# Optimization experiments

Measured on AMD Instinct MI355X. Metric: run time of the kernel, lower is better.

## Reference

```python
import jax, jax.numpy as jnp
import numpy as np
import math

B, L, D, H = 2, 2048, 1024, 16
DH = D // H  # 64


def setup_inputs() -> dict:
    key = jax.random.key(0)
    ks = jax.random.split(key, 8)
    s = 1.0 / math.sqrt(D)
    return {
        "query": jax.random.normal(ks[0], (B, L, D), dtype=jnp.float32),
        "key": jax.random.normal(ks[1], (B, L, D), dtype=jnp.float32),
        "value": jax.random.normal(ks[2], (B, L, D), dtype=jnp.float32),
        "attn_mask": jax.random.bernoulli(ks[3], 0.1, (B, L, L)),  # True = masked
        "Wq": jax.random.normal(ks[4], (D, D), dtype=jnp.float32) * s,
        "Wk": jax.random.normal(ks[5], (D, D), dtype=jnp.float32) * s,
        "Wv": jax.random.normal(ks[6], (D, D), dtype=jnp.float32) * s,
        "Wo": jax.random.normal(ks[7], (D, D), dtype=jnp.float32) * s,
    }


def reference(query, key, value, attn_mask, Wq, Wk, Wv, Wo):
    # torch nn.Linear computes x @ W.T (bias=False here)
    def shape(x):
        b, l, _ = x.shape
        return x.reshape(b, l, H, DH).transpose(0, 2, 1, 3)  # [B,H,L,DH]

    q = shape(query @ Wq.T) / jnp.sqrt(jnp.float32(DH))
    k = shape(key @ Wk.T)
    v = shape(value @ Wv.T)

    scores = jnp.einsum("bhqd,bhkd->bhqk", q, k)  # [B,H,Q,K]
    if attn_mask is not None:
        scores = jnp.where(attn_mask[:, None, :, :], jnp.float32(-1e18), scores)
    attn = jax.nn.softmax(scores, axis=-1)
    # dropout p=0.0 (eval/deterministic) -> identity
    context = jnp.einsum("bhqk,bhkd->bhqd", attn, v)
    context = context.transpose(0, 2, 1, 3).reshape(query.shape[0], -1, D)
    output = context @ Wo.T
    top_attn = attn[:, 0, :, :]
    return output, top_attn
```

## Files before the change

kernel.cpp:

```cpp
#include <hip/hip_runtime.h>

#define BB 2
#define LL 2048
#define DD 1024
#define HH 16
#define DHH 64

typedef _Float16 f16;
typedef _Float16 f16x8 __attribute__((ext_vector_type(8)));
typedef _Float16 f16x4 __attribute__((ext_vector_type(4)));
typedef _Float16 f16x2 __attribute__((ext_vector_type(2)));
typedef float f32x4 __attribute__((ext_vector_type(4)));
typedef unsigned long long u64;

#define VWAIT(N) asm volatile("s_waitcnt vmcnt(" #N ")" ::: "memory")
#define SB0() __builtin_amdgcn_sched_barrier(0)

__device__ __forceinline__ void gload_lds16(const void* g, void* l) {
    __builtin_amdgcn_global_load_lds(
        (const __attribute__((address_space(1))) void*)g,
        (__attribute__((address_space(3))) void*)l, 16, 0, 0);
}

__device__ __forceinline__ f16x4 cvt4f(float4 v) {
    f16x4 o;
    o[0] = (f16)v.x; o[1] = (f16)v.y; o[2] = (f16)v.z; o[3] = (f16)v.w;
    return o;
}

__global__ void prep(const float* __restrict__ q, const float* __restrict__ k,
                     const float* __restrict__ v, const int* __restrict__ msk,
                     const float* __restrict__ wq, const float* __restrict__ wk,
                     const float* __restrict__ wv, const float* __restrict__ wo,
                     f16* __restrict__ bufQ, f16* __restrict__ bufK, f16* __restrict__ bufV,
                     f16* __restrict__ wh, u64* __restrict__ Mp, float scq) {
    const int tid = threadIdx.x;
    const int y = blockIdx.y;
    if (y == 0) {
        const int lane = tid & 63;
        int w = (blockIdx.x * 256 + tid) >> 6;
        const int nw = (1024 * 256) >> 6;
        for (; w < BB * LL * 32; w += nw) {
            int mv = msk[(size_t)w * 64 + lane];
            u64 bits = __ballot(mv != 0);
            if (lane == 0) {
                const int kt = w & 31;
                const int bq = w >> 5;
                const int qq = bq & 2047, b = bq >> 11;
                Mp[((size_t)b * 32 + kt) * LL + qq] = bits;
            }
        }
    } else if (y == 1) {
        int i = blockIdx.x * 256 + tid;
        const int stride = 1024 * 256;
        for (; i < 4 * 262144; i += stride) {
            const int sel = i >> 18, j = i & 262143;
            const float* s = sel == 0 ? wq : sel == 1 ? wk : sel == 2 ? wv : wo;
            ((f16x4*)wh)[i] = cvt4f(((const float4*)s)[j]);
        }
    } else {
        const float* s = y == 2 ? q : y == 3 ? k : v;
        f16* o = y == 2 ? bufQ : y == 3 ? bufK : bufV;
        const float sc = y == 2 ? scq : 1.0f;
        int i = blockIdx.x * 256 + tid;
        const int stride = 1024 * 256;
        for (; i < (int)(BB * LL * DD / 4); i += stride) {
            float4 vv = ((const float4*)s)[i];
            vv.x *= sc; vv.y *= sc; vv.z *= sc; vv.w *= sc;
            ((f16x4*)o)[i] = cvt4f(vv);
        }
    }
}

__global__ void cvt_kernel(const float* __restrict__ src, f16* __restrict__ dst, int n4, float sc) {
    int i = blockIdx.x * blockDim.x + threadIdx.x;
    const int stride = gridDim.x * blockDim.x;
    for (; i < n4; i += stride) {
        float4 v = ((const float4*)src)[i];
        v.x *= sc; v.y *= sc; v.z *= sc; v.w *= sc;
        ((f16x4*)dst)[i] = cvt4f(v);
    }
}
__global__ void cvt4_kernel(const float* __restrict__ a, const float* __restrict__ b,
                            const float* __restrict__ c, const float* __restrict__ d,
                            f16* __restrict__ dst, int n4) {
    const float* s = blockIdx.y == 0 ? a : blockIdx.y == 1 ? b : blockIdx.y == 2 ? c : d;
    f16* o = dst + (size_t)blockIdx.y * n4 * 4;
    int i = blockIdx.x * blockDim.x + threadIdx.x;
    const int stride = gridDim.x * blockDim.x;
    for (; i < n4; i += stride)
        ((f16x4*)o)[i] = cvt4f(((const float4*)s)[i]);
}
__global__ void pack_mask(const int* __restrict__ mask, u64* __restrict__ out, int nwords) {
    const int lane = threadIdx.x & 63;
    int w = (blockIdx.x * blockDim.x + threadIdx.x) >> 6;
    const int nw = (gridDim.x * blockDim.x) >> 6;
    for (; w < nwords; w += nw) {
        int mv = mask[(size_t)w * 64 + lane];
        u64 bits = __ballot(mv != 0);
        if (lane == 0) {
            const int kt = w & 31;
            const int bq = w >> 5;
            const int qq = bq & 2047, b = bq >> 11;
            out[((size_t)b * 32 + kt) * LL + qq] = bits;
        }
    }
}

__device__ __forceinline__ void gemm_core(const f16* __restrict__ A, const f16* __restrict__ W,
                                          f16* __restrict__ C, int z, int xb, int yb, char* lds) {
    const int tid = threadIdx.x, wid = tid >> 6, lane = tid & 63;
    const int m0 = yb * 128, n0 = xb * 128;
    const int lq = lane & 15, lg = lane >> 4;
    const int wm = (wid >> 1) << 6, wn = (wid & 1) << 6;
    f32x4 acc[4][4] = {};

    #pragma unroll
    for (int t = 0; t < 2; ++t)
        #pragma unroll
        for (int j = 0; j < 2; ++j) {
            const int ldsoff = (wid * 2 + j) << 10;
            const int o = ldsoff + lane * 16;
            const int row = o >> 6, c8 = (o >> 4) & 3;
            gload_lds16(A + (size_t)(m0 + row) * DD + t * 32 + c8 * 8, lds + t * 8192 + ldsoff);
            gload_lds16(W + (size_t)(n0 + row) * DD + t * 32 + c8 * 8, lds + 24576 + t * 8192 + ldsoff);
        }

    for (int kt = 0; kt < 32; ++kt) {
        VWAIT(4);
        SB0();
        __builtin_amdgcn_s_barrier();
        SB0();
        {
            const int nk = (kt + 2 < 32) ? kt + 2 : 31;
            const int nb = (kt + 2) % 3;
            #pragma unroll
            for (int j = 0; j < 2; ++j) {
                const int ldsoff = (wid * 2 + j) << 10;
                const int o = ldsoff + lane * 16;
                const int row = o >> 6, c8 = (o >> 4) & 3;
                gload_lds16(A + (size_t)(m0 + row) * DD + nk * 32 + c8 * 8,
                            lds + nb * 8192 + ldsoff);
                gload_lds16(W + (size_t)(n0 + row) * DD + nk * 32 + c8 * 8,
                            lds + 24576 + nb * 8192 + ldsoff);
            }
        }
        SB0();

        const int cb = kt % 3;
        const char* Ab = lds + cb * 8192;
        const char* Bb = lds + 24576 + cb * 8192;
        f16x8 af[4], bf[4];
        #pragma unroll
        for (int m = 0; m < 4; ++m)
            af[m] = *(const f16x8*)(Ab + (wm + m * 16 + lq) * 64 + lg * 16);
        #pragma unroll
        for (int n = 0; n < 4; ++n)
            bf[n] = *(const f16x8*)(Bb + (wn + n * 16 + lq) * 64 + lg * 16);
        __builtin_amdgcn_s_setprio(1);
        #pragma unroll
        for (int m = 0; m < 4; ++m)
            #pragma unroll
            for (int n = 0; n < 4; ++n)
                acc[m][n] = __builtin_amdgcn_mfma_f32_16x16x32_f16(af[m], bf[n], acc[m][n], 0, 0, 0);
        __builtin_amdgcn_s_setprio(0);
    }

    #pragma unroll
    for (int m = 0; m < 4; ++m)
        #pragma unroll
        for (int n = 0; n < 4; ++n)
            #pragma unroll
            for (int r = 0; r < 4; ++r) {
                const int row = m0 + wm + m * 16 + lg * 4 + r;
                const int col = n0 + wn + n * 16 + lq;
                const float val = acc[m][n][r];
                if (z < 2) {
                    C[(size_t)row * DD + col] = (f16)val;
                } else {
                    const int b = row >> 11, l = row & 2047;
                    const int h = col >> 6, dh = col & 63;
                    C[((size_t)((b * HH + h) * DHH + dh) << 11) + l] = (f16)val;
                }
            }
}

__global__ __launch_bounds__(256) void gemm_qkv(
        const f16* __restrict__ A0, const f16* __restrict__ A1, const f16* __restrict__ A2,
        const f16* __restrict__ W0, const f16* __restrict__ W1, const f16* __restrict__ W2,
        f16* __restrict__ C0, f16* __restrict__ C1, f16* __restrict__ C2) {
    __shared__ __align__(16) char lds[49152];
    const int bid = blockIdx.x;
    const int xcd = bid & 7, j = bid >> 3;
    const int p = xcd * 12 + (j >> 3);
    const int xb = j & 7;
    const int z = p >> 5, yb = p & 31;
    const f16* A = z == 0 ? A0 : z == 1 ? A1 : A2;
    const f16* W = z == 0 ? W0 : z == 1 ? W1 : W2;
    f16* C       = z == 0 ? C0 : z == 1 ? C1 : C2;
    gemm_core(A, W, C, z, xb, yb, lds);
}

__global__ __launch_bounds__(256) void gemm_one(const f16* __restrict__ A, const f16* __restrict__ W,
                                                f16* __restrict__ C, int z) {
    __shared__ __align__(16) char lds[49152];
    gemm_core(A, W, C, z, blockIdx.x, blockIdx.y, lds);
}

__global__ __launch_bounds__(256) void gemm_out(const f16* __restrict__ A, const f16* __restrict__ W,
                                                float* __restrict__ C) {
    __shared__ __align__(16) char lds[36864];
    const int bid = blockIdx.x;
    const int xcd = bid & 7, j = bid >> 3;
    const int yb = xcd * 4 + (j >> 4);
    const int xb = j & 15;
    const int tid = threadIdx.x, wid = tid >> 6, lane = tid & 63;
    const int m0 = yb * 128, n0 = xb * 64;
    const int lq = lane & 15, lg = lane >> 4;
    const int wm = wid * 32;
    f32x4 acc[2][4] = {};

    #pragma unroll
    for (int t = 0; t < 2; ++t) {
        #pragma unroll
        for (int j2 = 0; j2 < 2; ++j2) {
            const int o = (j2 * 256 + tid) * 16;
            const int row = o >> 6, c8 = (o >> 4) & 3;
            gload_lds16(A + (size_t)(m0 + row) * DD + t * 32 + c8 * 8,
                        lds + t * 8192 + j2 * 4096 + (wid << 10));
        }
        {
            const int o = tid * 16;
            const int row = o >> 6, c8 = (o >> 4) & 3;
            gload_lds16(W + (size_t)(n0 + row) * DD + t * 32 + c8 * 8,
                        lds + 24576 + t * 4096 + (wid << 10));
        }
    }

    for (int kt = 0; kt < 32; ++kt) {
        VWAIT(3);
        SB0();
        __builtin_amdgcn_s_barrier();
        SB0();
        {
            const int nk = (kt + 2 < 32) ? kt + 2 : 31;
            const int nb = (kt + 2) % 3;
            #pragma unroll
            for (int j2 = 0; j2 < 2; ++j2) {
                const int o = (j2 * 256 + tid) * 16;
                const int row = o >> 6, c8 = (o >> 4) & 3;
                gload_lds16(A + (size_t)(m0 + row) * DD + nk * 32 + c8 * 8,
                            lds + nb * 8192 + j2 * 4096 + (wid << 10));
            }
            {
                const int o = tid * 16;
                const int row = o >> 6, c8 = (o >> 4) & 3;
                gload_lds16(W + (size_t)(n0 + row) * DD + nk * 32 + c8 * 8,
                            lds + 24576 + nb * 4096 + (wid << 10));
            }
        }
        SB0();

        const int cb = kt % 3;
        const char* Ab = lds + cb * 8192;
        const char* Bb = lds + 24576 + cb * 4096;
        f16x8 af[2], bf[4];
        #pragma unroll
        for (int m = 0; m < 2; ++m)
            af[m] = *(const f16x8*)(Ab + (wm + m * 16 + lq) * 64 + lg * 16);
        #pragma unroll
        for (int n = 0; n < 4; ++n)
            bf[n] = *(const f16x8*)(Bb + (n * 16 + lq) * 64 + lg * 16);
        __builtin_amdgcn_s_setprio(1);
        #pragma unroll
        for (int m = 0; m < 2; ++m)
            #pragma unroll
            for (int n = 0; n < 4; ++n)
                acc[m][n] = __builtin_amdgcn_mfma_f32_16x16x32_f16(af[m], bf[n], acc[m][n], 0, 0, 0);
        __builtin_amdgcn_s_setprio(0);
    }

    #pragma unroll
    for (int m = 0; m < 2; ++m)
        #pragma unroll
        for (int n = 0; n < 4; ++n)
            #pragma unroll
            for (int r = 0; r < 4; ++r) {
                const int row = m0 + wm + m * 16 + lg * 4 + r;
                const int col = n0 + n * 16 + lq;
                C[(size_t)row * DD + col] = acc[m][n][r];
            }
}

template<bool TOPF16>
__global__ __launch_bounds__(256) void attn_fwd(const f16* __restrict__ Qp, const f16* __restrict__ Kp,
                                                const f16* __restrict__ VTp,
                                                const u64* __restrict__ Mp,
                                                f16* __restrict__ Op, void* __restrict__ topout,
                                                float* __restrict__ statsLinv) {
    extern __shared__ char lds[];
    const int tid = threadIdx.x, wid = tid >> 6, lane = tid & 63;
    const int lq = lane & 15, lg = lane >> 4;
    const int bid = blockIdx.x;
    const int xcd = bid & 7, j = bid >> 3;
    const int bh = xcd * 4 + (j >> 5);
    const int qt = j & 31;
    const int b = bh >> 4, h = bh & 15;
    const bool topblk = (h == 0);
    const int qrow = qt * 64 + wid * 16 + lq;

    f16x8 qf[2];
    #pragma unroll
    for (int kk = 0; kk < 2; ++kk)
        qf[kk] = *(const f16x8*)(Qp + (size_t)(b * LL + qrow) * DD + h * 64 + (kk * 4 + lg) * 8);

    {
        #pragma unroll
        for (int jj = 0; jj < 2; ++jj) {
            const int o = (wid * 2 + jj) * 1024 + lane * 16;
            const int row = o >> 7, sc = ((o >> 4) & 7) ^ (row & 7);
            gload_lds16(Kp + (size_t)(b * LL + row) * DD + h * 64 + sc * 8,
                        lds + 8192 + (wid * 2 + jj) * 1024);
            gload_lds16(VTp + (size_t)((b * HH + h) * DHH + row) * LL + sc * 8,
                        lds + 24576 + (wid * 2 + jj) * 1024);
        }
    }

    float lsum = 0.f;
    f32x4 acc[4] = {};

    for (int kt = 0; kt < 32; ++kt) {
        if (topblk && kt > 0) { VWAIT(4); } else { VWAIT(0); }
        SB0();
        __builtin_amdgcn_s_barrier();
        SB0();
        const u64 cm = Mp[((size_t)b * 32 + kt) * LL + qrow];
        SB0();
        {
            const int nk = (kt + 1 < 32) ? kt + 1 : 31;
            const int nb = (kt + 1) & 1;
            #pragma unroll
            for (int jj = 0; jj < 2; ++jj) {
                const int o = (wid * 2 + jj) * 1024 + lane * 16;
                const int row = o >> 7, sc = ((o >> 4) & 7) ^ (row & 7);
                gload_lds16(Kp + (size_t)(b * LL + nk * 64 + row) * DD + h * 64 + sc * 8,
                            lds + 8192 + nb * 8192 + (wid * 2 + jj) * 1024);
                gload_lds16(VTp + (size_t)((b * HH + h) * DHH + row) * LL + nk * 64 + sc * 8,
                            lds + 24576 + nb * 8192 + (wid * 2 + jj) * 1024);
            }
        }
        SB0();

        const int cb = kt & 1;
        const char* Kb = lds + 8192 + cb * 8192;
        const char* Vb = lds + 24576 + cb * 8192;

        f32x4 s[4] = {};
        __builtin_amdgcn_s_setprio(1);
        #pragma unroll
        for (int f = 0; f < 4; ++f)
            #pragma unroll
            for (int kk = 0; kk < 2; ++kk) {
                const int co = (((kk * 4 + lg) ^ (lq & 7)) << 4);
                f16x8 kf = *(const f16x8*)(Kb + (f * 16 + lq) * 128 + co);
                s[f] = __builtin_amdgcn_mfma_f32_16x16x32_f16(kf, qf[kk], s[f], 0, 0, 0);
            }
        __builtin_amdgcn_s_setprio(0);

        const u64 wsh = cm >> (lg * 4);
        const unsigned lo = (unsigned)wsh, hi = (unsigned)(wsh >> 32);
        f16x4 ph[4];
        #pragma unroll
        for (int f = 0; f < 4; ++f) {
            const unsigned nib = ((f < 2) ? (lo >> (f * 16)) : (hi >> ((f - 2) * 16))) & 0xFu;
            #pragma unroll
            for (int r = 0; r < 4; ++r)
                if (nib & (1u << r)) s[f][r] = -1e18f;
            const float p0 = __builtin_amdgcn_exp2f(s[f][0]);
            const float p1 = __builtin_amdgcn_exp2f(s[f][1]);
            const float p2 = __builtin_amdgcn_exp2f(s[f][2]);
            const float p3 = __builtin_amdgcn_exp2f(s[f][3]);
            lsum += (p0 + p1) + (p2 + p3);
            f16x2 pa = __builtin_bit_cast(f16x2, __builtin_amdgcn_cvt_pkrtz(p0, p1));
            f16x2 pb = __builtin_bit_cast(f16x2, __builtin_amdgcn_cvt_pkrtz(p2, p3));
            ph[f][0] = pa[0]; ph[f][1] = pa[1]; ph[f][2] = pb[0]; ph[f][3] = pb[1];
        }

        if (topblk) {
            if (TOPF16) {
                f16* T = (f16*)topout;
                #pragma unroll
                for (int f = 0; f < 4; ++f)
                    *(f16x4*)(T + ((size_t)b * LL + qrow) * LL + kt * 64 + f * 16 + lg * 4) = ph[f];
            } else {
                float* T = (float*)topout;
                #pragma unroll
                for (int f = 0; f < 4; ++f)
                    *(f32x4*)(T + ((size_t)b * LL + qrow) * LL + kt * 64 + f * 16 + lg * 4) = s[f];
            }
        }

        #pragma unroll
        for (int f = 0; f < 4; ++f) {
            const int chunk = f * 2 + (lg >> 1);
            const int bo = ((chunk ^ (lq & 7)) << 4) + (lg & 1) * 8;
            *(f16x4*)(lds + (wid << 11) + lq * 128 + bo) = ph[f];
        }

        __builtin_amdgcn_s_setprio(1);
        #pragma unroll
        for (int kk = 0; kk < 2; ++kk) {
            const int co = (((kk * 4 + lg) ^ (lq & 7)) << 4);
            f16x8 pf = *(const f16x8*)(lds + (wid << 11) + lq * 128 + co);
            #pragma unroll
            for (int f = 0; f < 4; ++f) {
                f16x8 vf = *(const f16x8*)(Vb + (f * 16 + lq) * 128 + co);
                acc[f] = __builtin_amdgcn_mfma_f32_16x16x32_f16(vf, pf, acc[f], 0, 0, 0);
            }
        }
        __builtin_amdgcn_s_setprio(0);
    }

    lsum += __shfl_xor(lsum, 16);
    lsum += __shfl_xor(lsum, 32);
    const float linv = 1.f / lsum;
    #pragma unroll
    for (int f = 0; f < 4; ++f) {
        f16x4 ov;
        #pragma unroll
        for (int r = 0; r < 4; ++r) ov[r] = (f16)(acc[f][r] * linv);
        *(f16x4*)(Op + (size_t)(b * LL + qrow) * DD + h * 64 + f * 16 + lg * 4) = ov;
    }
    if (topblk && lg == 0) statsLinv[(size_t)b * LL + qrow] = linv;
}

template<bool TOPF16>
__global__ void norm_top(float* __restrict__ top, const void* __restrict__ src,
                         const float* __restrict__ linvp, int n) {
    int i = blockIdx.x * blockDim.x + threadIdx.x;
    const int stride = gridDim.x * blockDim.x;
    if (TOPF16) {
        const f16x8* s8 = (const f16x8*)src;
        for (; i < n; i += stride) {
            f16x8 v = s8[i];
            const float linv = linvp[(i * 8) >> 11];
            float4 a, bq;
            a.x = (float)v[0] * linv; a.y = (float)v[1] * linv;
            a.z = (float)v[2] * linv; a.w = (float)v[3] * linv;
            bq.x = (float)v[4] * linv; bq.y = (float)v[5] * linv;
            bq.z = (float)v[6] * linv; bq.w = (float)v[7] * linv;
            ((float4*)top)[i * 2] = a;
            ((float4*)top)[i * 2 + 1] = bq;
        }
    } else {
        for (; i < n; i += stride) {
            float4 v = ((const float4*)top)[i];
            const float linv = linvp[(i * 4) >> 11];
            v.x = __builtin_amdgcn_exp2f(v.x) * linv;
            v.y = __builtin_amdgcn_exp2f(v.y) * linv;
            v.z = __builtin_amdgcn_exp2f(v.z) * linv;
            v.w = __builtin_amdgcn_exp2f(v.w) * linv;
            ((float4*)top)[i] = v;
        }
    }
}

extern "C" void kernel_launch(void* const* d_in, const int* in_sizes, int n_in,
                              void* d_out, int out_size, void* d_ws, size_t ws_size,
                              hipStream_t stream) {
    const float* q   = (const float*)d_in[0];
    const float* k   = (const float*)d_in[1];
    const float* v   = (const float*)d_in[2];
    const int*   msk = (const int*)d_in[3];
    const float* wq  = (const float*)d_in[4];
    const float* wk  = (const float*)d_in[5];
    const float* wv  = (const float*)d_in[6];
    const float* wo  = (const float*)d_in[7];
    float* out = (float*)d_out;

    const size_t NX = (size_t)BB * LL * DD;
    const size_t NW = (size_t)DD * DD;
    const int NMW = BB * LL * (LL / 64);
    const size_t NXo = NX;
    const float SCQ = 0.125f * 1.4426950408889634f;
    const int ALDS = 40960;

    f16* ws = (f16*)d_ws;
    const size_t needed = (6 * NX + 4 * NW) * 2 + (size_t)NMW * 8 + (size_t)BB * LL * 4;
    const bool fused = ws_size >= needed;

    if (fused) {
        f16* bufQ = ws;
        f16* bufK = bufQ + NX;
        f16* bufV = bufK + NX;
        f16* topP = bufK;
        f16* wh   = bufV + NX;
        f16* wqh = wh, *wkh = wh + NW, *wvh = wh + 2 * NW, *woh = wh + 3 * NW;
        f16* Qp  = wh + 4 * NW;
        f16* Kp  = Qp + NX;
        f16* VTp = Kp + NX;
        u64* Mp  = (u64*)(VTp + NX);
        float* statsLinv = (float*)(Mp + NMW);

        prep<<<dim3(1024, 5), 256, 0, stream>>>(q, k, v, msk, wq, wk, wv, wo,
                                                bufQ, bufK, bufV, wh, Mp, SCQ);
        gemm_qkv<<<768, 256, 0, stream>>>(bufQ, bufK, bufV, wqh, wkh, wvh, Qp, Kp, VTp);
        attn_fwd<true><<<1024, 256, ALDS, stream>>>(Qp, Kp, VTp, Mp, bufQ, topP, statsLinv);
        norm_top<true><<<2048, 256, 0, stream>>>(out + NXo, topP, statsLinv,
                                                 (int)((size_t)BB * LL * LL / 8));
        gemm_out<<<512, 256, 0, stream>>>(bufQ, woh, out);
    } else {
        f16* bufA = ws;
        f16* wh   = bufA + NX;
        f16* wqh = wh, *wkh = wh + NW, *wvh = wh + 2 * NW, *woh = wh + 3 * NW;
        f16* Qp  = wh + 4 * NW;
        f16* Kp  = Qp + NX;
        f16* VTp = Kp + NX;
        u64* Mp  = (u64*)(VTp + NX);
        float* statsLinv = (float*)(Mp + NMW);

        pack_mask<<<256, 256, 0, stream>>>(msk, Mp, NMW);
        cvt4_kernel<<<dim3(128, 4), 256, 0, stream>>>(wq, wk, wv, wo, wh, (int)(NW / 4));
        cvt_kernel<<<2048, 256, 0, stream>>>(q, bufA, (int)(NX / 4), SCQ);
        gemm_one<<<dim3(8, 32), 256, 0, stream>>>(bufA, wqh, Qp, 0);
        cvt_kernel<<<2048, 256, 0, stream>>>(k, bufA, (int)(NX / 4), 1.f);
        gemm_one<<<dim3(8, 32), 256, 0, stream>>>(bufA, wkh, Kp, 1);
        cvt_kernel<<<2048, 256, 0, stream>>>(v, bufA, (int)(NX / 4), 1.f);
        gemm_one<<<dim3(8, 32), 256, 0, stream>>>(bufA, wvh, VTp, 2);
        attn_fwd<false><<<1024, 256, ALDS, stream>>>(Qp, Kp, VTp, Mp, bufA,
                                                     out + NXo, statsLinv);
        norm_top<false><<<2048, 256, 0, stream>>>(out + NXo, out + NXo, statsLinv,
                                                  (int)((size_t)BB * LL * LL / 4));
        gemm_out<<<512, 256, 0, stream>>>(bufA, woh, out);
    }
}
```

Baseline: 167.0 us.

## Fuse fp32-to-fp16 input conversion into QKV GEMM and merge norm_top with output GEMM

```diff
diff --git a/kernel.cpp b/kernel.cpp
--- a/kernel.cpp
+++ b/kernel.cpp
@@ -14,6 +14,7 @@
 typedef unsigned long long u64;
 
 #define VWAIT(N) asm volatile("s_waitcnt vmcnt(" #N ")" ::: "memory")
+#define LWAIT0() asm volatile("s_waitcnt lgkmcnt(0)" ::: "memory")
 #define SB0() __builtin_amdgcn_sched_barrier(0)
 
 __device__ __forceinline__ void gload_lds16(const void* g, void* l) {
@@ -28,15 +29,23 @@
     return o;
 }
 
-__global__ void prep(const float* __restrict__ q, const float* __restrict__ k,
-                     const float* __restrict__ v, const int* __restrict__ msk,
+__device__ __forceinline__ f16x8 cvt8f(float4 a, float4 b) {
+    f16x2 p0 = __builtin_bit_cast(f16x2, __builtin_amdgcn_cvt_pkrtz(a.x, a.y));
+    f16x2 p1 = __builtin_bit_cast(f16x2, __builtin_amdgcn_cvt_pkrtz(a.z, a.w));
+    f16x2 p2 = __builtin_bit_cast(f16x2, __builtin_amdgcn_cvt_pkrtz(b.x, b.y));
+    f16x2 p3 = __builtin_bit_cast(f16x2, __builtin_amdgcn_cvt_pkrtz(b.z, b.w));
+    f16x8 r;
+    r[0] = p0[0]; r[1] = p0[1]; r[2] = p1[0]; r[3] = p1[1];
+    r[4] = p2[0]; r[5] = p2[1]; r[6] = p3[0]; r[7] = p3[1];
+    return r;
+}
+
+__global__ void prep(const int* __restrict__ msk,
                      const float* __restrict__ wq, const float* __restrict__ wk,
                      const float* __restrict__ wv, const float* __restrict__ wo,
-                     f16* __restrict__ bufQ, f16* __restrict__ bufK, f16* __restrict__ bufV,
-                     f16* __restrict__ wh, u64* __restrict__ Mp, float scq) {
+                     f16* __restrict__ wh, u64* __restrict__ Mp) {
     const int tid = threadIdx.x;
-    const int y = blockIdx.y;
-    if (y == 0) {
+    if (blockIdx.y == 0) {
         const int lane = tid & 63;
         int w = (blockIdx.x * 256 + tid) >> 6;
         const int nw = (1024 * 256) >> 6;
@@ -50,24 +59,13 @@
                 Mp[((size_t)b * 32 + kt) * LL + qq] = bits;
             }
         }
-    } else if (y == 1) {
+    } else {
         int i = blockIdx.x * 256 + tid;
         const int stride = 1024 * 256;
         for (; i < 4 * 262144; i += stride) {
             const int sel = i >> 18, j = i & 262143;
             const float* s = sel == 0 ? wq : sel == 1 ? wk : sel == 2 ? wv : wo;
             ((f16x4*)wh)[i] = cvt4f(((const float4*)s)[j]);
-        }
-    } else {
-        const float* s = y == 2 ? q : y == 3 ? k : v;
-        f16* o = y == 2 ? bufQ : y == 3 ? bufK : bufV;
-        const float sc = y == 2 ? scq : 1.0f;
-        int i = blockIdx.x * 256 + tid;
-        const int stride = 1024 * 256;
-        for (; i < (int)(BB * LL * DD / 4); i += stride) {
-            float4 vv = ((const float4*)s)[i];
-            vv.x *= sc; vv.y *= sc; vv.z *= sc; vv.w *= sc;
-            ((f16x4*)o)[i] = cvt4f(vv);
         }
     }
 }
@@ -107,19 +105,164 @@
     }
 }
 
-__device__ __forceinline__ void gemm_core(const f16* __restrict__ A, const f16* __restrict__ W,
-                                          f16* __restrict__ C, int z, int xb, int yb, char* lds) {
+__global__ __launch_bounds__(256) void gemm_qkv(
+        const float* __restrict__ A0, const float* __restrict__ A1, const float* __restrict__ A2,
+        const f16* __restrict__ W0, const f16* __restrict__ W1, const f16* __restrict__ W2,
+        f16* __restrict__ C0, f16* __restrict__ C1, f16* __restrict__ C2, float scq) {
+    __shared__ __align__(16) char lds[49152];
+    const int bid = blockIdx.x;
+    const int xcd = bid & 7, j = bid >> 3;
+    const int p = xcd * 12 + (j >> 3);
+    const int xb = j & 7;
+    const int z = p >> 5, yb = p & 31;
+    const float* __restrict__ A = z == 0 ? A0 : z == 1 ? A1 : A2;
+    const f16* __restrict__ W = z == 0 ? W0 : z == 1 ? W1 : W2;
+    f16* __restrict__ C       = z == 0 ? C0 : z == 1 ? C1 : C2;
+
     const int tid = threadIdx.x, wid = tid >> 6, lane = tid & 63;
     const int m0 = yb * 128, n0 = xb * 128;
     const int lq = lane & 15, lg = lane >> 4;
     const int wm = (wid >> 1) << 6, wn = (wid & 1) << 6;
+    const int ar0 = (wid * 2) * 16 + (lane >> 2);
+    const int ar1 = (wid * 2 + 1) * 16 + (lane >> 2);
+    const int ac8 = lane & 3;
+    const float* a0p = A + (size_t)(m0 + ar0) * DD + ac8 * 8;
+    const float* a1p = A + (size_t)(m0 + ar1) * DD + ac8 * 8;
+    char* aw0 = lds + ar0 * 64 + ac8 * 16;
+    char* aw1 = lds + ar1 * 64 + ac8 * 16;
+
     f32x4 acc[4][4] = {};
+    float4 arA[2][2], arB[2][2];
+
+    {
+        float4 t00 = *(const float4*)(a0p + 0 * 32);
+        float4 t01 = *(const float4*)(a0p + 0 * 32 + 4);
+        float4 t10 = *(const float4*)(a1p + 0 * 32);
+        float4 t11 = *(const float4*)(a1p + 0 * 32 + 4);
+        VWAIT(0);
+        *(f16x8*)(aw0 + 0 * 8192) = cvt8f(t00, t01);
+        *(f16x8*)(aw1 + 0 * 8192) = cvt8f(t10, t11);
+        t00 = *(const float4*)(a0p + 1 * 32);
+        t01 = *(const float4*)(a0p + 1 * 32 + 4);
+        t10 = *(const float4*)(a1p + 1 * 32);
+        t11 = *(const float4*)(a1p + 1 * 32 + 4);
+        VWAIT(0);
+        *(f16x8*)(aw0 + 1 * 8192) = cvt8f(t00, t01);
+        *(f16x8*)(aw1 + 1 * 8192) = cvt8f(t10, t11);
+        SB0();
+        arA[0][0] = *(const float4*)(a0p + 2 * 32);
+        arA[0][1] = *(const float4*)(a0p + 2 * 32 + 4);
+        arA[1][0] = *(const float4*)(a1p + 2 * 32);
+        arA[1][1] = *(const float4*)(a1p + 2 * 32 + 4);
+        SB0();
+        #pragma unroll
+        for (int t = 0; t < 2; ++t)
+            #pragma unroll
+            for (int jj = 0; jj < 2; ++jj) {
+                const int ldsoff = (wid * 2 + jj) << 10;
+                const int o = ldsoff + lane * 16;
+                const int row = o >> 6, c8 = (o >> 4) & 3;
+                gload_lds16(W + (size_t)(n0 + row) * DD + t * 32 + c8 * 8,
+                            lds + 24576 + t * 8192 + ldsoff);
+            }
+        LWAIT0();
+    }
+
+    #pragma unroll
+    for (int kt = 0; kt < 32; ++kt) {
+        VWAIT(2);
+        SB0();
+        __builtin_amdgcn_s_barrier();
+        SB0();
+        {
+            const int wb = (kt + 2) % 3;
+            const int nk = (kt + 3 < 32) ? kt + 3 : 31;
+            if ((kt & 1) == 0) {
+                *(f16x8*)(aw0 + wb * 8192) = cvt8f(arA[0][0], arA[0][1]);
+                *(f16x8*)(aw1 + wb * 8192) = cvt8f(arA[1][0], arA[1][1]);
+                SB0();
+                arB[0][0] = *(const float4*)(a0p + nk * 32);
+                arB[0][1] = *(const float4*)(a0p + nk * 32 + 4);
+                arB[1][0] = *(const float4*)(a1p + nk * 32);
+                arB[1][1] = *(const float4*)(a1p + nk * 32 + 4);
+            } else {
+                *(f16x8*)(aw0 + wb * 8192) = cvt8f(arB[0][0], arB[0][1]);
+                *(f16x8*)(aw1 + wb * 8192) = cvt8f(arB[1][0], arB[1][1]);
+                SB0();
+                arA[0][0] = *(const float4*)(a0p + nk * 32);
+                arA[0][1] = *(const float4*)(a0p + nk * 32 + 4);
+                arA[1][0] = *(const float4*)(a1p + nk * 32);
+                arA[1][1] = *(const float4*)(a1p + nk * 32 + 4);
+            }
+        }
+        SB0();
+        {
+            const int nk = (kt + 2 < 32) ? kt + 2 : 31;
+            const int nb = (kt + 2) % 3;
+            #pragma unroll
+            for (int jj = 0; jj < 2; ++jj) {
+                const int ldsoff = (wid * 2 + jj) << 10;
+                const int o = ldsoff + lane * 16;
+                const int row = o >> 6, c8 = (o >> 4) & 3;
+                gload_lds16(W + (size_t)(n0 + row) * DD + nk * 32 + c8 * 8,
+                            lds + 24576 + nb * 8192 + ldsoff);
+            }
+        }
+        SB0();
+
+        const int cb = kt % 3;
+        const char* Ab = lds + cb * 8192;
+        const char* Bb = lds + 24576 + cb * 8192;
+        f16x8 af[4], bf[4];
+        #pragma unroll
+        for (int m = 0; m < 4; ++m)
+            af[m] = *(const f16x8*)(Ab + (wm + m * 16 + lq) * 64 + lg * 16);
+        #pragma unroll
+        for (int n = 0; n < 4; ++n)
+            bf[n] = *(const f16x8*)(Bb + (wn + n * 16 + lq) * 64 + lg * 16);
+        __builtin_amdgcn_s_setprio(1);
+        #pragma unroll
+        for (int m = 0; m < 4; ++m)
+            #pragma unroll
+            for (int n = 0; n < 4; ++n)
+                acc[m][n] = __builtin_amdgcn_mfma_f32_16x16x32_f16(af[m], bf[n], acc[m][n], 0, 0, 0);
+        __builtin_amdgcn_s_setprio(0);
+    }
+
+    const float oscale = (z == 0) ? scq : 1.0f;
+    #pragma unroll
+    for (int m = 0; m < 4; ++m)
+        #pragma unroll
+        for (int n = 0; n < 4; ++n)
+            #pragma unroll
+            for (int r = 0; r < 4; ++r) {
+                const int row = m0 + wm + m * 16 + lg * 4 + r;
+                const int col = n0 + wn + n * 16 + lq;
+                const float val = acc[m][n][r] * oscale;
+                if (z < 2) {
+                    C[(size_t)row * DD + col] = (f16)val;
+                } else {
+                    const int b = row >> 11, l = row & 2047;
+                    const int h = col >> 6, dh = col & 63;
+                    C[((size_t)((b * HH + h) * DHH + dh) << 11) + l] = (f16)val;
+                }
+            }
+}
+
+__global__ __launch_bounds__(256) void gemm_one(const f16* __restrict__ A, const f16* __restrict__ W,
+                                                f16* __restrict__ C, int z) {
+    __shared__ __align__(16) char lds[49152];
+    const int tid = threadIdx.x, wid = tid >> 6, lane = tid & 63;
+    const int m0 = blockIdx.y * 128, n0 = blockIdx.x * 128;
+    const int lq = lane & 15, lg = lane >> 4;
+    const int wm = (wid >> 1) << 6, wn = (wid & 1) << 6;
+    f32x4 acc[4][4] = {};
 
     #pragma unroll
     for (int t = 0; t < 2; ++t)
         #pragma unroll
-        for (int j = 0; j < 2; ++j) {
-            const int ldsoff = (wid * 2 + j) << 10;
+        for (int jj = 0; jj < 2; ++jj) {
+            const int ldsoff = (wid * 2 + jj) << 10;
             const int o = ldsoff + lane * 16;
             const int row = o >> 6, c8 = (o >> 4) & 3;
             gload_lds16(A + (size_t)(m0 + row) * DD + t * 32 + c8 * 8, lds + t * 8192 + ldsoff);
@@ -135,8 +278,8 @@
             const int nk = (kt + 2 < 32) ? kt + 2 : 31;
             const int nb = (kt + 2) % 3;
             #pragma unroll
-            for (int j = 0; j < 2; ++j) {
-                const int ldsoff = (wid * 2 + j) << 10;
+            for (int jj = 0; jj < 2; ++jj) {
+                const int ldsoff = (wid * 2 + jj) << 10;
                 const int o = ldsoff + lane * 16;
                 const int row = o >> 6, c8 = (o >> 4) & 3;
                 gload_lds16(A + (size_t)(m0 + row) * DD + nk * 32 + c8 * 8,
@@ -185,36 +328,49 @@
             }
 }
 
-__global__ __launch_bounds__(256) void gemm_qkv(
-        const f16* __restrict__ A0, const f16* __restrict__ A1, const f16* __restrict__ A2,
-        const f16* __restrict__ W0, const f16* __restrict__ W1, const f16* __restrict__ W2,
-        f16* __restrict__ C0, f16* __restrict__ C1, f16* __restrict__ C2) {
-    __shared__ __align__(16) char lds[49152];
-    const int bid = blockIdx.x;
-    const int xcd = bid & 7, j = bid >> 3;
-    const int p = xcd * 12 + (j >> 3);
-    const int xb = j & 7;
-    const int z = p >> 5, yb = p & 31;
-    const f16* A = z == 0 ? A0 : z == 1 ? A1 : A2;
-    const f16* W = z == 0 ? W0 : z == 1 ? W1 : W2;
-    f16* C       = z == 0 ? C0 : z == 1 ? C1 : C2;
-    gemm_core(A, W, C, z, xb, yb, lds);
-}
-
-__global__ __launch_bounds__(256) void gemm_one(const f16* __restrict__ A, const f16* __restrict__ W,
-                                                f16* __restrict__ C, int z) {
-    __shared__ __align__(16) char lds[49152];
-    gemm_core(A, W, C, z, blockIdx.x, blockIdx.y, lds);
-}
-
-__global__ __launch_bounds__(256) void gemm_out(const f16* __restrict__ A, const f16* __restrict__ W,
-                                                float* __restrict__ C) {
+template<bool TOPF16>
+__global__ __launch_bounds__(256) void finale(const f16* __restrict__ A, const f16* __restrict__ W,
+                                              float* __restrict__ C, float* __restrict__ top,
+                                              const void* __restrict__ src,
+                                              const float* __restrict__ linvp) {
     __shared__ __align__(16) char lds[36864];
+    const int tid = threadIdx.x;
+    if (blockIdx.x >= 512) {
+        int i = (blockIdx.x - 512) * 256 + tid;
+        const int stride = 1024 * 256;
+        if (TOPF16) {
+            const f16x8* s8 = (const f16x8*)src;
+            const int n = (int)((size_t)BB * LL * LL / 8);
+            for (; i < n; i += stride) {
+                f16x8 v = s8[i];
+                const float linv = linvp[(i * 8) >> 11];
+                float4 a, bq;
+                a.x = (float)v[0] * linv; a.y = (float)v[1] * linv;
+                a.z = (float)v[2] * linv; a.w = (float)v[3] * linv;
+                bq.x = (float)v[4] * linv; bq.y = (float)v[5] * linv;
+                bq.z = (float)v[6] * linv; bq.w = (float)v[7] * linv;
+                ((float4*)top)[i * 2] = a;
+                ((float4*)top)[i * 2 + 1] = bq;
+            }
+        } else {
+            const int n = (int)((size_t)BB * LL * LL / 4);
+            for (; i < n; i += stride) {
+                float4 v = ((const float4*)top)[i];
+                const float linv = linvp[(i * 4) >> 11];
+                v.x = __builtin_amdgcn_exp2f(v.x) * linv;
+                v.y = __builtin_amdgcn_exp2f(v.y) * linv;
+                v.z = __builtin_amdgcn_exp2f(v.z) * linv;
+                v.w = __builtin_amdgcn_exp2f(v.w) * linv;
+                ((float4*)top)[i] = v;
+            }
+        }
+        return;
+    }
     const int bid = blockIdx.x;
     const int xcd = bid & 7, j = bid >> 3;
     const int yb = xcd * 4 + (j >> 4);
     const int xb = j & 15;
-    const int tid = threadIdx.x, wid = tid >> 6, lane = tid & 63;
+    const int wid = tid >> 6, lane = tid & 63;
     const int m0 = yb * 128, n0 = xb * 64;
     const int lq = lane & 15, lg = lane >> 4;
     const int wm = wid * 32;
@@ -434,37 +590,6 @@
     if (topblk && lg == 0) statsLinv[(size_t)b * LL + qrow] = linv;
 }
 
-template<bool TOPF16>
-__global__ void norm_top(float* __restrict__ top, const void* __restrict__ src,
-                         const float* __restrict__ linvp, int n) {
-    int i = blockIdx.x * blockDim.x + threadIdx.x;
-    const int stride = gridDim.x * blockDim.x;
-    if (TOPF16) {
-        const f16x8* s8 = (const f16x8*)src;
-        for (; i < n; i += stride) {
-            f16x8 v = s8[i];
-            const float linv = linvp[(i * 8) >> 11];
-            float4 a, bq;
-            a.x = (float)v[0] * linv; a.y = (float)v[1] * linv;
-            a.z = (float)v[2] * linv; a.w = (float)v[3] * linv;
-            bq.x = (float)v[4] * linv; bq.y = (float)v[5] * linv;
-            bq.z = (float)v[6] * linv; bq.w = (float)v[7] * linv;
-            ((float4*)top)[i * 2] = a;
-            ((float4*)top)[i * 2 + 1] = bq;
-        }
-    } else {
-        for (; i < n; i += stride) {
-            float4 v = ((const float4*)top)[i];
-            const float linv = linvp[(i * 4) >> 11];
-            v.x = __builtin_amdgcn_exp2f(v.x) * linv;
-            v.y = __builtin_amdgcn_exp2f(v.y) * linv;
-            v.z = __builtin_amdgcn_exp2f(v.z) * linv;
-            v.w = __builtin_amdgcn_exp2f(v.w) * linv;
-            ((float4*)top)[i] = v;
-        }
-    }
-}
-
 extern "C" void kernel_launch(void* const* d_in, const int* in_sizes, int n_in,
                               void* d_out, int out_size, void* d_ws, size_t ws_size,
                               hipStream_t stream) {
@@ -490,25 +615,20 @@
     const bool fused = ws_size >= needed;
 
     if (fused) {
-        f16* bufQ = ws;
-        f16* bufK = bufQ + NX;
-        f16* bufV = bufK + NX;
-        f16* topP = bufK;
-        f16* wh   = bufV + NX;
+        f16* Op   = ws;
+        f16* wh   = Op + NX;
         f16* wqh = wh, *wkh = wh + NW, *wvh = wh + 2 * NW, *woh = wh + 3 * NW;
         f16* Qp  = wh + 4 * NW;
         f16* Kp  = Qp + NX;
         f16* VTp = Kp + NX;
-        u64* Mp  = (u64*)(VTp + NX);
+        f16* topP = VTp + NX;
+        u64* Mp  = (u64*)(topP + 2 * NX);
         float* statsLinv = (float*)(Mp + NMW);
 
-        prep<<<dim3(1024, 5), 256, 0, stream>>>(q, k, v, msk, wq, wk, wv, wo,
-                                                bufQ, bufK, bufV, wh, Mp, SCQ);
-        gemm_qkv<<<768, 256, 0, stream>>>(bufQ, bufK, bufV, wqh, wkh, wvh, Qp, Kp, VTp);
-        attn_fwd<true><<<1024, 256, ALDS, stream>>>(Qp, Kp, VTp, Mp, bufQ, topP, statsLinv);
-        norm_top<true><<<2048, 256, 0, stream>>>(out + NXo, topP, statsLinv,
-                                                 (int)((size_t)BB * LL * LL / 8));
-        gemm_out<<<512, 256, 0, stream>>>(bufQ, woh, out);
+        prep<<<dim3(1024, 2), 256, 0, stream>>>(msk, wq, wk, wv, wo, wh, Mp);
+        gemm_qkv<<<768, 256, 0, stream>>>(q, k, v, wqh, wkh, wvh, Qp, Kp, VTp, SCQ);
+        attn_fwd<true><<<1024, 256, ALDS, stream>>>(Qp, Kp, VTp, Mp, Op, topP, statsLinv);
+        finale<true><<<1536, 256, 0, stream>>>(Op, woh, out, out + NXo, topP, statsLinv);
     } else {
         f16* bufA = ws;
         f16* wh   = bufA + NX;
@@ -529,8 +649,6 @@
         gemm_one<<<dim3(8, 32), 256, 0, stream>>>(bufA, wvh, VTp, 2);
         attn_fwd<false><<<1024, 256, ALDS, stream>>>(Qp, Kp, VTp, Mp, bufA,
                                                      out + NXo, statsLinv);
-        norm_top<false><<<2048, 256, 0, stream>>>(out + NXo, out + NXo, statsLinv,
-                                                  (int)((size_t)BB * LL * LL / 4));
-        gemm_out<<<512, 256, 0, stream>>>(bufA, woh, out);
-    }
-}
+        finale<false><<<1536, 256, 0, stream>>>(bufA, woh, out, out + NXo, out + NXo, statsLinv);
+    }
+}
```

New measurement: 155.4 us, median of 2. 6.9% less time.
